# Kernel tuning notes

Measured on AMD Instinct MI355X. Metric: run time of the kernel, lower is better.

Reference implementation:

```python
import jax
import jax.numpy as jnp
import numpy as np

VOCAB = 16384
WIDTH = 256
BETA = 0.25
EPS = 1e-12  # F.normalize eps


def setup_inputs() -> dict:
    key = jax.random.key(0)
    k1, k2, k3 = jax.random.split(key, 3)
    class_tokens = jax.random.normal(k1, (32, 1, WIDTH), dtype=jnp.float32)
    patch_tokens = jax.random.normal(k2, (32, WIDTH, 16, 16), dtype=jnp.float32)
    W = jax.random.normal(k3, (VOCAB, WIDTH), dtype=jnp.float32) * 0.02  # codebook
    return {"class_tokens": class_tokens, "patch_tokens": patch_tokens, "W": W}


def _l2norm(x):
    return x / jnp.maximum(jnp.linalg.norm(x, axis=-1, keepdims=True), EPS)


def reference(class_tokens, patch_tokens, W):
    B, L, C = class_tokens.shape
    _, _, H, Wd = patch_tokens.shape
    # (B,C,H,W) -> (B,HW,C)
    pt = patch_tokens.reshape(B, C, H * Wd).transpose(0, 2, 1)
    NxC = jnp.concatenate([class_tokens, pt], axis=1).reshape(-1, C)  # [N,C]

    # vocab_norm branch: cosine-similarity argmax on detached, normalized vectors
    xn = _l2norm(jax.lax.stop_gradient(NxC))      # [N,C]
    Wn = _l2norm(W)                                # [V,C] (column-normalized W.T)
    sim = xn @ Wn.T                                # [N,V] big matmul
    idx = jnp.argmax(sim, axis=1)                  # [N]

    counts = jnp.zeros((VOCAB,), jnp.float32).at[idx].add(1.0)  # bincount

    fhat_g = W[idx]                                # codebook gather [N,C]
    vq_loss = BETA * jnp.mean((jax.lax.stop_gradient(fhat_g) - NxC) ** 2) \
              + jnp.mean((fhat_g - jax.lax.stop_gradient(NxC)) ** 2)

    # straight-through estimator
    fhat = jax.lax.stop_gradient(fhat_g - NxC) + NxC

    prob = counts / counts.sum()
    vocab_usage = jnp.mean((prob > 0.01 / VOCAB).astype(jnp.float32)) * 100.0

    fhat = fhat.reshape(B, L + H * Wd, C)
    fhat_class = fhat[:, :L, :]
    fhat_patch = fhat[:, L:, :].reshape(B, H, Wd, C).transpose(0, 3, 1, 2)
    return fhat_class, fhat_patch, vq_loss, vocab_usage
```

## Files before the change

kernel.cpp:

```cpp
#include <hip/hip_runtime.h>
#include <stdint.h>

#define VOCAB 16384
#define NB 32
#define NTOK 8224
#define MTILES 65
#define MP 8320
#define NBY 128
#define TILE_BYTES 65536
#define NLOSS 2056
#define MWIN 2.25e-3f
#define TOKCHUNKS 520

typedef _Float16 half8 __attribute__((ext_vector_type(8)));
typedef float f4 __attribute__((ext_vector_type(4)));
typedef __attribute__((address_space(1))) const uint32_t* gas_t;
typedef __attribute__((address_space(3))) uint32_t* las_t;

__device__ __forceinline__ void async16(const void* g, void* l) {
    __builtin_amdgcn_global_load_lds((gas_t)g, (las_t)l, 16, 0, 0);
}

__device__ __forceinline__ unsigned long long key64(float v, int idx) {
    unsigned u = __float_as_uint(v);
    u = (u & 0x80000000u) ? ~u : (u | 0x80000000u);
    return ((unsigned long long)u << 32) | (unsigned)(~idx);
}

__device__ __forceinline__ float keyval(unsigned long long k) {
    unsigned u = (unsigned)(k >> 32);
    u = (u & 0x80000000u) ? (u & 0x7fffffffu) : ~u;
    return __uint_as_float(u);
}

__device__ __forceinline__ void merge2(unsigned long long& k1, unsigned long long& k2,
                                       unsigned long long p1, unsigned long long p2) {
    unsigned long long lo = k1 < p1 ? k1 : p1;
    k1 = k1 > p1 ? k1 : p1;
    unsigned long long m2 = k2 > p2 ? k2 : p2;
    k2 = lo > m2 ? lo : m2;
}

__global__ __launch_bounds__(256) void k_prep(const float* __restrict__ patch, const float* __restrict__ W,
                                              float* __restrict__ tok, char* __restrict__ bpk,
                                              float* __restrict__ nwv, unsigned int* __restrict__ used) {
    __shared__ float buf[4290];
    __shared__ float pr[16][16];
    __shared__ float sn[16];
    int id = blockIdx.x;
    int tid = threadIdx.x;
    if (id < 512) {
        if (id == 0) {
            for (int i = tid; i < VOCAB / 32; i += 256) used[i] = 0u;
        }
        int c0 = (id & 3) * 64, p0 = ((id >> 2) & 3) * 64, b = id >> 4;
        int l = tid & 63, w = tid >> 6;
        const float* src = patch + b * 65536;
#pragma unroll
        for (int i = 0; i < 16; ++i) {
            int row = i * 4 + w;
            buf[row * 65 + l] = src[(c0 + row) * 256 + p0 + l];
        }
        __syncthreads();
#pragma unroll
        for (int i = 0; i < 16; ++i) {
            int prow = i * 4 + w;
            tok[(b * 257 + 1 + p0 + prow) * 256 + c0 + l] = buf[l * 65 + prow];
        }
    } else {
        int g = id - 512;
        int row0 = g * 16;
        int rr = tid >> 4, cb = tid & 15;
        const float* sp = W + (size_t)(row0 + rr) * 256 + cb * 16;
        float psum = 0.0f;
#pragma unroll
        for (int i = 0; i < 4; ++i) {
            float4 v = *(const float4*)(sp + i * 4);
            *(float4*)&buf[rr * 264 + cb * 16 + i * 4] = v;
            psum += v.x * v.x + v.y * v.y + v.z * v.z + v.w * v.w;
        }
        pr[rr][cb] = psum;
        __syncthreads();
        if (tid < 16) {
            float s = 0.0f;
#pragma unroll
            for (int j = 0; j < 16; ++j) s += pr[tid][j];
            float nv = fmaxf(sqrtf(s), 1e-12f);
            sn[tid] = nv;
            nwv[row0 + tid] = nv;
        }
        __syncthreads();
        int c = tid & 63, pair = tid >> 6;
        int m = c & 15, jb = (c >> 4) * 8;
        float inv = 1.0f / sn[m];
        char* base = bpk + (size_t)(g >> 3) * TILE_BYTES + (size_t)(g & 7) * 1024 + c * 16;
#pragma unroll
        for (int it = 0; it < 2; ++it) {
            int k32 = it * 4 + pair;
            const float* rowp = &buf[m * 264 + k32 * 32 + jb];
            half8 o;
#pragma unroll
            for (int j = 0; j < 8; ++j) o[j] = (_Float16)(rowp[j] * inv);
            *(half8*)(base + (size_t)k32 * 8192) = o;
        }
    }
}

__global__ __launch_bounds__(256) void k_packA(const float* __restrict__ tok, const float* __restrict__ cls,
                                               char* __restrict__ apk, float* __restrict__ ntokv) {
    __shared__ float t[16][264];
    __shared__ float pr[16][16];
    __shared__ float sn[16];
    int g = blockIdx.x;
    int row0 = g * 16;
    int tid = threadIdx.x;
    int rr = tid >> 4, cb = tid & 15;
    int grow = row0 + rr;
    int b = grow / 257, s = grow - b * 257;
    const float* sp = (s == 0 && grow < NTOK) ? (cls + (size_t)b * 256 + cb * 16)
                                              : (tok + (size_t)grow * 256 + cb * 16);
    float psum = 0.0f;
#pragma unroll
    for (int i = 0; i < 4; ++i) {
        float4 v = (grow < NTOK) ? *(const float4*)(sp + i * 4) : make_float4(0.f, 0.f, 0.f, 0.f);
        *(float4*)&t[rr][cb * 16 + i * 4] = v;
        psum += v.x * v.x + v.y * v.y + v.z * v.z + v.w * v.w;
    }
    pr[rr][cb] = psum;
    __syncthreads();
    if (tid < 16) {
        float s2 = 0.0f;
#pragma unroll
        for (int j = 0; j < 16; ++j) s2 += pr[tid][j];
        float nv = fmaxf(sqrtf(s2), 1e-12f);
        sn[tid] = nv;
        ntokv[row0 + tid] = nv;
    }
    __syncthreads();
    int c = tid & 63, pair = tid >> 6;
    int m = c & 15, jb = (c >> 4) * 8;
    float inv = 1.0f / sn[m];
    char* base = apk + (size_t)(g >> 3) * TILE_BYTES + (size_t)(g & 7) * 1024 + c * 16;
#pragma unroll
    for (int it = 0; it < 2; ++it) {
        int k32 = it * 4 + pair;
        const float* rowp = &t[m][k32 * 32 + jb];
        half8 o;
#pragma unroll
        for (int j = 0; j < 8; ++j) o[j] = (_Float16)(rowp[j] * inv);
        *(half8*)(base + (size_t)k32 * 8192) = o;
    }
}

__global__ __launch_bounds__(256) void k_sim(const char* __restrict__ apk, const char* __restrict__ bpk,
                                             unsigned long long* __restrict__ pb) {
    __shared__ char lds[65536];
    int id = blockIdx.x;
    int xcd = id & 7, r = id >> 3;
    int st = r / 104, within = r % 104;
    int stid = xcd * 10 + st;
    int sx = stid % 5, sy = stid / 5;
    int bx = sx * 13 + within % 13;
    int by = sy * 8 + within / 13;

    int tid = threadIdx.x;
    int ln = tid & 63, wv = tid >> 6;
    int mh = wv >> 1, nh = wv & 1;
    const char* abase = apk + (size_t)bx * TILE_BYTES;
    const half8* Bg = (const half8*)(bpk + (size_t)by * TILE_BYTES);

    f4 acc[4][4];
#pragma unroll
    for (int i = 0; i < 4; ++i)
#pragma unroll
        for (int j = 0; j < 4; ++j) acc[i][j] = (f4){0.f, 0.f, 0.f, 0.f};

    half8 b0[2][4], b1[2][4];
#define LOADB(DST, P)                                                                 \
    _Pragma("unroll")                                                                 \
    for (int s = 0; s < 2; ++s)                                                       \
        _Pragma("unroll")                                                             \
        for (int ni = 0; ni < 4; ++ni)                                                \
            DST[s][ni] = Bg[((P) * 16 + s * 8 + nh * 4 + ni) * 64 + ln];

#define FRAGS(P)                                                                      \
    half8 ah[2][4];                                                                   \
    _Pragma("unroll")                                                                 \
    for (int s = 0; s < 2; ++s) {                                                     \
        const half8* Af = (const half8*)(lds + (P) * 16384 + s * 8192);               \
        _Pragma("unroll")                                                             \
        for (int mi = 0; mi < 4; ++mi) ah[s][mi] = Af[(mh * 4 + mi) * 64 + ln];       \
    }

#define DOMFMA(BH)                                                                    \
    __builtin_amdgcn_s_setprio(1);                                                    \
    _Pragma("unroll")                                                                 \
    for (int s = 0; s < 2; ++s)                                                       \
        _Pragma("unroll")                                                             \
        for (int mi = 0; mi < 4; ++mi)                                                \
            _Pragma("unroll")                                                         \
            for (int ni = 0; ni < 4; ++ni)                                            \
                acc[mi][ni] = __builtin_amdgcn_mfma_f32_16x16x32_f16(BH[s][ni], ah[s][mi], acc[mi][ni], 0, 0, 0); \
    __builtin_amdgcn_s_setprio(0);

    LOADB(b0, 0);
#pragma unroll
    for (int i = 0; i < 16; ++i) {
        int c = wv * 16 + i;
        async16(abase + (c << 10) + (ln << 4), lds + (c << 10));
    }
    LOADB(b1, 1);
    __syncthreads();

    { FRAGS(0); DOMFMA(b0); }
    __builtin_amdgcn_sched_barrier(0);
    { LOADB(b0, 2); FRAGS(1); DOMFMA(b1); }
    __builtin_amdgcn_sched_barrier(0);
    { LOADB(b1, 3); FRAGS(2); DOMFMA(b0); }
    __builtin_amdgcn_sched_barrier(0);
    { FRAGS(3); DOMFMA(b1); }

    __syncthreads();
    unsigned long long* s1 = (unsigned long long*)lds;
    unsigned long long* s2 = (unsigned long long*)(lds + 2048);

    int col = ln & 15, quad = ln >> 4;
    unsigned qb = (unsigned)(3 - quad) << 4;
    int nbase0 = by * 128 + nh * 64;
#pragma unroll
    for (int mi = 0; mi < 4; ++mi) {
        float v1 = -3.0f, v2 = -3.5f;
#pragma unroll
        for (int ni = 0; ni < 4; ++ni)
#pragma unroll
            for (int rg = 0; rg < 4; ++rg) {
                unsigned e = 15u - (unsigned)(ni * 4 + rg);
                float pv = __uint_as_float((__float_as_uint(acc[mi][ni][rg]) & 0xFFFFFFF0u) | e);
                v2 = __builtin_amdgcn_fmed3f(v1, v2, pv);
                v1 = fmaxf(v1, pv);
            }
        float w1 = __uint_as_float((__float_as_uint(v1) & 0xFFFFFFCFu) | qb);
        float w2 = __uint_as_float((__float_as_uint(v2) & 0xFFFFFFCFu) | qb);
        v1 = fmaxf(w1, w2);
        v2 = fminf(w1, w2);
#pragma unroll
        for (int off = 16; off < 64; off <<= 1) {
            float p1 = __shfl_xor(v1, off);
            float p2 = __shfl_xor(v2, off);
            v2 = __builtin_amdgcn_fmed3f(v1, p1, fmaxf(v2, p2));
            v1 = fmaxf(v1, p1);
        }
        if (quad == 0) {
            unsigned u1 = __float_as_uint(v1), u2 = __float_as_uint(v2);
            int q1 = 3 - (int)((u1 >> 4) & 3u), o1 = 15 - (int)(u1 & 15u);
            int q2 = 3 - (int)((u2 >> 4) & 3u), o2 = 15 - (int)(u2 & 15u);
            int n1 = ((o1 >> 2) << 4) + q1 * 4 + (o1 & 3);
            int n2 = ((o2 >> 2) << 4) + q2 * 4 + (o2 & 3);
            int row = mh * 64 + mi * 16 + col;
            s1[row * 2 + nh] = key64(v1, nbase0 + n1);
            s2[row * 2 + nh] = key64(v2, nbase0 + n2);
        }
    }
    __syncthreads();
    if (tid < 128) {
        unsigned long long k1 = s1[tid * 2], k2 = s2[tid * 2];
        merge2(k1, k2, s1[tid * 2 + 1], s2[tid * 2 + 1]);
        ulonglong2 v; v.x = k1; v.y = k2;
        ((ulonglong2*)pb)[((size_t)(bx * 128 + tid)) * 128 + by] = v;
    }
#undef LOADB
#undef FRAGS
#undef DOMFMA
}

__global__ __launch_bounds__(256) void k_gather(const unsigned long long* __restrict__ pb,
                                                const float* __restrict__ W, const float* __restrict__ tok,
                                                const float* __restrict__ cls,
                                                const float* __restrict__ ntok, const float* __restrict__ nw,
                                                float* __restrict__ out, int* __restrict__ idxbuf,
                                                float* __restrict__ lossbuf, unsigned int* __restrict__ used) {
    __shared__ float lp[4];
    int tid = threadIdx.x;
    int t = blockIdx.x * 4 + (tid >> 6);
    int ln = tid & 63, w = tid >> 6;
    const ulonglong2* pv = (const ulonglong2*)pb;
    ulonglong2 ea = pv[(size_t)t * 128 + ln];
    ulonglong2 eb = pv[(size_t)t * 128 + 64 + ln];
    unsigned long long g = ea.x > eb.x ? ea.x : eb.x;
#pragma unroll
    for (int off = 1; off < 64; off <<= 1) {
        unsigned long long o = __shfl_xor(g, off);
        if (o > g) g = o;
    }
    float T = keyval(g) - MWIN;
    int tq = t / 257, ts = t - tq * 257;
    const float* xrow = (ts == 0) ? (cls + (size_t)tq * 256) : (tok + (size_t)t * 256);
    f4 xv = *(const f4*)&xrow[ln * 4];
    unsigned long long k4[4] = {ea.x, ea.y, eb.x, eb.y};
    unsigned long long msk[4];
    int total = 0;
#pragma unroll
    for (int gi = 0; gi < 4; ++gi) {
        msk[gi] = __ballot(keyval(k4[gi]) >= T);
        total += __popcll(msk[gi]);
    }
    int besti;
    if (total == 1) {
        unsigned long long ck = 0;
#pragma unroll
        for (int gi = 0; gi < 4; ++gi)
            if (msk[gi]) { int src = __ffsll(msk[gi]) - 1; ck = __shfl(k4[gi], src); }
        besti = (int)(~(unsigned)(ck & 0xffffffffu));
    } else {
        float nt = ntok[t];
        float bestv = -3.0f;
        besti = 0x7fffffff;
#pragma unroll
        for (int gi = 0; gi < 4; ++gi) {
            unsigned long long mask = msk[gi];
            while (mask) {
                int src = __ffsll(mask) - 1;
                mask &= mask - 1;
                unsigned long long ck = __shfl(k4[gi], src);
                int ci = (int)(~(unsigned)(ck & 0xffffffffu));
                f4 wc = *(const f4*)&W[(size_t)ci * 256 + ln * 4];
                float d = xv.x * wc.x + xv.y * wc.y + xv.z * wc.z + xv.w * wc.w;
#pragma unroll
                for (int off = 1; off < 64; off <<= 1) d += __shfl_xor(d, off);
                float sim = d / (nt * nw[ci]);
                if (sim > bestv || (sim == bestv && ci < besti)) { bestv = sim; besti = ci; }
            }
        }
    }
    int bi = besti;
    f4 wr = *(const f4*)&W[(size_t)bi * 256 + ln * 4];
    float dx = wr.x - xv.x, dy = wr.y - xv.y, dz = wr.z - xv.z, dw = wr.w - xv.w;
    float ls = dx * dx + dy * dy + dz * dz + dw * dw;
#pragma unroll
    for (int off = 1; off < 64; off <<= 1) ls += __shfl_xor(ls, off);
    if (ln == 0) {
        lp[w] = ls;
        atomicOr(&used[bi >> 5], 1u << (bi & 31));
        idxbuf[t] = bi;
    }
    if (ts == 0) {
        *(f4*)&out[tq * 256 + ln * 4] = wr;
    }
    __syncthreads();
    if (tid == 0) lossbuf[blockIdx.x] = lp[0] + lp[1] + lp[2] + lp[3];
}

__global__ __launch_bounds__(256) void k_scatter(const int* __restrict__ idxbuf, const float* __restrict__ W,
                                                 float* __restrict__ out, const unsigned int* __restrict__ used,
                                                 const float* __restrict__ lossbuf) {
    __shared__ float t64[64][65];
    __shared__ int sidx[64];
    int c0 = blockIdx.x * 64, p0 = blockIdx.y * 64, b = blockIdx.z;
    int tid = threadIdx.x;
    if (tid < 64) sidx[tid] = idxbuf[b * 257 + 1 + p0 + tid];
    __syncthreads();
    int l = tid & 63, w = tid >> 6;
#pragma unroll
    for (int i = 0; i < 16; ++i) {
        int p = i * 4 + w;
        t64[p][l] = W[(size_t)sidx[p] * 256 + c0 + l];
    }
    __syncthreads();
#pragma unroll
    for (int i = 0; i < 16; ++i) {
        int c = i * 4 + w;
        out[8192 + (size_t)b * 65536 + (size_t)(c0 + c) * 256 + p0 + l] = t64[l][c];
    }
    if (blockIdx.x == 0 && blockIdx.y == 0 && blockIdx.z == 0) {
        int cnt = 0;
        float ls = 0.0f;
        for (int i = tid; i < VOCAB / 32; i += 256) cnt += __popc(used[i]);
        for (int i = tid; i < NLOSS; i += 256) ls += lossbuf[i];
#pragma unroll
        for (int off = 32; off > 0; off >>= 1) {
            cnt += __shfl_down(cnt, off);
            ls += __shfl_down(ls, off);
        }
        __shared__ int p4f[4];
        __shared__ float f4s[4];
        if ((tid & 63) == 0) { p4f[tid >> 6] = cnt; f4s[tid >> 6] = ls; }
        __syncthreads();
        if (tid == 0) {
            int c = p4f[0] + p4f[1] + p4f[2] + p4f[3];
            float lsum = f4s[0] + f4s[1] + f4s[2] + f4s[3];
            out[8192 + 2097152] = 1.25f * lsum / (float)(NTOK * 256);
            out[8192 + 2097152 + 1] = 100.0f * (float)c / (float)VOCAB;
        }
    }
}

extern "C" void kernel_launch(void* const* d_in, const int* in_sizes, int n_in,
                              void* d_out, int out_size, void* d_ws, size_t ws_size,
                              hipStream_t stream) {
    (void)in_sizes; (void)n_in; (void)out_size; (void)ws_size;
    const float* cls = (const float*)d_in[0];
    const float* patch = (const float*)d_in[1];
    const float* W = (const float*)d_in[2];
    float* out = (float*)d_out;

    char* ws = (char*)d_ws;
    float* tok = (float*)ws;
    char* apk = ws + (size_t)NTOK * 256 * 4;
    char* bpk = apk + (size_t)MTILES * TILE_BYTES;
    unsigned long long* pb = (unsigned long long*)(bpk + (size_t)NBY * TILE_BYTES);
    float* ntokv = (float*)(pb + (size_t)MP * NBY * 2);
    float* nwv = ntokv + MP;
    float* lossbuf = nwv + VOCAB;
    int* idxbuf = (int*)(lossbuf + NLOSS);
    unsigned int* used = (unsigned int*)(idxbuf + NTOK);

    k_prep<<<1536, 256, 0, stream>>>(patch, W, tok, bpk, nwv, used);
    k_packA<<<TOKCHUNKS, 256, 0, stream>>>(tok, cls, apk, ntokv);
    k_sim<<<MTILES * NBY, 256, 0, stream>>>(apk, bpk, pb);
    k_gather<<<NLOSS, 256, 0, stream>>>(pb, W, tok, cls, ntokv, nwv, out, idxbuf, lossbuf, used);
    k_scatter<<<dim3(4, 4, NB), 256, 0, stream>>>(idxbuf, W, out, used, lossbuf);
}
```

Baseline: 186.3 us.

## Switch similarity GEMM to 32x32x16 MFMA with repacked operand layout

Replaces the 16x16x32 MFMA tiles in the similarity kernel with 32x32x16 MFMA, and repacks the A and B fp16 operands in the prep kernels into a matching 32-row fragment layout. The top-2 argmax epilogue is rewritten for the 32x32 accumulator lane mapping, which needs one cross-half shuffle instead of two. The larger MFMA does the same FLOPs with fewer instructions and fragment loads per tile. It costs more accumulator registers per instruction and relies on intricate index encoding in the low mantissa bits, which now uses 6 bits instead of 4 or 6 and could perturb near-tie argmax results.

After: 196.0 us. 1.05x slower.

```diff
diff --git a/kernel.cpp b/kernel.cpp
--- a/kernel.cpp
+++ b/kernel.cpp
@@ -14,6 +14,7 @@
 
 typedef _Float16 half8 __attribute__((ext_vector_type(8)));
 typedef float f4 __attribute__((ext_vector_type(4)));
+typedef float f16v __attribute__((ext_vector_type(16)));
 typedef __attribute__((address_space(1))) const uint32_t* gas_t;
 typedef __attribute__((address_space(3))) uint32_t* las_t;
 
@@ -40,6 +41,7 @@
     unsigned long long m2 = k2 > p2 ? k2 : p2;
     k2 = lo > m2 ? lo : m2;
 }
+
 
 __global__ __launch_bounds__(256) void k_prep(const float* __restrict__ patch, const float* __restrict__ W,
                                               float* __restrict__ tok, char* __restrict__ bpk,
@@ -93,15 +95,18 @@
         int c = tid & 63, pair = tid >> 6;
         int m = c & 15, jb = (c >> 4) * 8;
         float inv = 1.0f / sn[m];
-        char* base = bpk + (size_t)(g >> 3) * TILE_BYTES + (size_t)(g & 7) * 1024 + c * 16;
+        int rlow = (g & 1) * 16 + m;
+        int rb = (g >> 1) & 3;
+        char* tbase = bpk + (size_t)(g >> 3) * TILE_BYTES + rb * 1024;
 #pragma unroll
         for (int it = 0; it < 2; ++it) {
             int k32 = it * 4 + pair;
+            int oI = k32 * 4 + (c >> 4);
             const float* rowp = &buf[m * 264 + k32 * 32 + jb];
             half8 o;
 #pragma unroll
             for (int j = 0; j < 8; ++j) o[j] = (_Float16)(rowp[j] * inv);
-            *(half8*)(base + (size_t)k32 * 8192) = o;
+            *(half8*)(tbase + (size_t)(oI >> 1) * 4096 + (size_t)(rlow + 32 * (oI & 1)) * 16) = o;
         }
     }
 }
@@ -140,15 +145,18 @@
     int c = tid & 63, pair = tid >> 6;
     int m = c & 15, jb = (c >> 4) * 8;
     float inv = 1.0f / sn[m];
-    char* base = apk + (size_t)(g >> 3) * TILE_BYTES + (size_t)(g & 7) * 1024 + c * 16;
+    int rlow = (g & 1) * 16 + m;
+    int rb = (g >> 1) & 3;
+    char* tbase = apk + (size_t)(g >> 3) * TILE_BYTES + rb * 1024;
 #pragma unroll
     for (int it = 0; it < 2; ++it) {
         int k32 = it * 4 + pair;
+        int oI = k32 * 4 + (c >> 4);
         const float* rowp = &t[m][k32 * 32 + jb];
         half8 o;
 #pragma unroll
         for (int j = 0; j < 8; ++j) o[j] = (_Float16)(rowp[j] * inv);
-        *(half8*)(base + (size_t)k32 * 8192) = o;
+        *(half8*)(tbase + (size_t)(oI >> 1) * 4096 + (size_t)(rlow + 32 * (oI & 1)) * 16) = o;
     }
 }
 
@@ -169,38 +177,39 @@
     const char* abase = apk + (size_t)bx * TILE_BYTES;
     const half8* Bg = (const half8*)(bpk + (size_t)by * TILE_BYTES);
 
-    f4 acc[4][4];
-#pragma unroll
-    for (int i = 0; i < 4; ++i)
-#pragma unroll
-        for (int j = 0; j < 4; ++j) acc[i][j] = (f4){0.f, 0.f, 0.f, 0.f};
-
-    half8 b0[2][4], b1[2][4];
+    f16v acc[2][2];
+#pragma unroll
+    for (int i = 0; i < 2; ++i)
+#pragma unroll
+        for (int j = 0; j < 2; ++j)
+#pragma unroll
+            for (int e = 0; e < 16; ++e) acc[i][j][e] = 0.0f;
+
+    half8 b0[4][2], b1[4][2];
 #define LOADB(DST, P)                                                                 \
     _Pragma("unroll")                                                                 \
-    for (int s = 0; s < 2; ++s)                                                       \
+    for (int kk = 0; kk < 4; ++kk)                                                    \
         _Pragma("unroll")                                                             \
-        for (int ni = 0; ni < 4; ++ni)                                                \
-            DST[s][ni] = Bg[((P) * 16 + s * 8 + nh * 4 + ni) * 64 + ln];
+        for (int nt = 0; nt < 2; ++nt)                                                \
+            DST[kk][nt] = Bg[(((P) * 4 + kk) * 4 + nh * 2 + nt) * 64 + ln];
 
 #define FRAGS(P)                                                                      \
-    half8 ah[2][4];                                                                   \
+    half8 ah[4][2];                                                                   \
     _Pragma("unroll")                                                                 \
-    for (int s = 0; s < 2; ++s) {                                                     \
-        const half8* Af = (const half8*)(lds + (P) * 16384 + s * 8192);               \
+    for (int kk = 0; kk < 4; ++kk)                                                    \
         _Pragma("unroll")                                                             \
-        for (int mi = 0; mi < 4; ++mi) ah[s][mi] = Af[(mh * 4 + mi) * 64 + ln];       \
-    }
+        for (int tt = 0; tt < 2; ++tt)                                                \
+            ah[kk][tt] = *(const half8*)(lds + (size_t)(((P) * 4 + kk) * 4 + mh * 2 + tt) * 1024 + ln * 16);
 
 #define DOMFMA(BH)                                                                    \
     __builtin_amdgcn_s_setprio(1);                                                    \
     _Pragma("unroll")                                                                 \
-    for (int s = 0; s < 2; ++s)                                                       \
+    for (int kk = 0; kk < 4; ++kk)                                                    \
         _Pragma("unroll")                                                             \
-        for (int mi = 0; mi < 4; ++mi)                                                \
+        for (int tt = 0; tt < 2; ++tt)                                                \
             _Pragma("unroll")                                                         \
-            for (int ni = 0; ni < 4; ++ni)                                            \
-                acc[mi][ni] = __builtin_amdgcn_mfma_f32_16x16x32_f16(BH[s][ni], ah[s][mi], acc[mi][ni], 0, 0, 0); \
+            for (int nt = 0; nt < 2; ++nt)                                            \
+                acc[tt][nt] = __builtin_amdgcn_mfma_f32_32x32x16_f16(BH[kk][nt], ah[kk][tt], acc[tt][nt], 0, 0, 0); \
     __builtin_amdgcn_s_setprio(0);
 
     LOADB(b0, 0);
@@ -224,39 +233,38 @@
     unsigned long long* s1 = (unsigned long long*)lds;
     unsigned long long* s2 = (unsigned long long*)(lds + 2048);
 
-    int col = ln & 15, quad = ln >> 4;
-    unsigned qb = (unsigned)(3 - quad) << 4;
+    int colt = ln & 31, half = ln >> 5;
+    unsigned hb = (unsigned)(1 - half) << 5;
     int nbase0 = by * 128 + nh * 64;
 #pragma unroll
-    for (int mi = 0; mi < 4; ++mi) {
+    for (int tt = 0; tt < 2; ++tt) {
         float v1 = -3.0f, v2 = -3.5f;
 #pragma unroll
-        for (int ni = 0; ni < 4; ++ni)
-#pragma unroll
-            for (int rg = 0; rg < 4; ++rg) {
-                unsigned e = 15u - (unsigned)(ni * 4 + rg);
-                float pv = __uint_as_float((__float_as_uint(acc[mi][ni][rg]) & 0xFFFFFFF0u) | e);
+        for (int nt = 0; nt < 2; ++nt)
+#pragma unroll
+            for (int rg = 0; rg < 16; ++rg) {
+                unsigned e = 31u - (unsigned)(nt * 16 + rg);
+                float pv = __uint_as_float((__float_as_uint(acc[tt][nt][rg]) & 0xFFFFFFE0u) | e);
                 v2 = __builtin_amdgcn_fmed3f(v1, v2, pv);
                 v1 = fmaxf(v1, pv);
             }
-        float w1 = __uint_as_float((__float_as_uint(v1) & 0xFFFFFFCFu) | qb);
-        float w2 = __uint_as_float((__float_as_uint(v2) & 0xFFFFFFCFu) | qb);
+        float w1 = __uint_as_float((__float_as_uint(v1) & 0xFFFFFFDFu) | hb);
+        float w2 = __uint_as_float((__float_as_uint(v2) & 0xFFFFFFDFu) | hb);
         v1 = fmaxf(w1, w2);
         v2 = fminf(w1, w2);
-#pragma unroll
-        for (int off = 16; off < 64; off <<= 1) {
-            float p1 = __shfl_xor(v1, off);
-            float p2 = __shfl_xor(v2, off);
+        {
+            float p1 = __shfl_xor(v1, 32);
+            float p2 = __shfl_xor(v2, 32);
             v2 = __builtin_amdgcn_fmed3f(v1, p1, fmaxf(v2, p2));
             v1 = fmaxf(v1, p1);
         }
-        if (quad == 0) {
+        if (half == 0) {
             unsigned u1 = __float_as_uint(v1), u2 = __float_as_uint(v2);
-            int q1 = 3 - (int)((u1 >> 4) & 3u), o1 = 15 - (int)(u1 & 15u);
-            int q2 = 3 - (int)((u2 >> 4) & 3u), o2 = 15 - (int)(u2 & 15u);
-            int n1 = ((o1 >> 2) << 4) + q1 * 4 + (o1 & 3);
-            int n2 = ((o2 >> 2) << 4) + q2 * 4 + (o2 & 3);
-            int row = mh * 64 + mi * 16 + col;
+            int sA = 31 - (int)(u1 & 31u), hA = 1 - (int)((u1 >> 5) & 1u);
+            int sB = 31 - (int)(u2 & 31u), hB = 1 - (int)((u2 >> 5) & 1u);
+            int n1 = (sA >> 4) * 32 + ((sA & 15) & 3) + 8 * ((sA & 15) >> 2) + 4 * hA;
+            int n2 = (sB >> 4) * 32 + ((sB & 15) & 3) + 8 * ((sB & 15) >> 2) + 4 * hB;
+            int row = mh * 64 + tt * 32 + colt;
             s1[row * 2 + nh] = key64(v1, nbase0 + n1);
             s2[row * 2 + nh] = key64(v2, nbase0 + n2);
         }
```
